# Kernel optimization log

Hardware: AMD Instinct MI355X
Metric: run time of the kernel (lower is better)

Reference implementation:

```python
import jax, jax.numpy as jnp
import numpy as np

N, IN, OUT = 8192, 4096, 4096
GROUP = 4
ACT_BITS = 8


def setup_inputs() -> dict:
    key = jax.random.key(0)
    k_x, k_w, k_b = jax.random.split(key, 3)
    input = jax.random.normal(k_x, (N, IN), dtype=jnp.float32)
    # ternary weights in {-1, 0, +1}, stored as float for compute
    weight = jax.random.randint(k_w, (OUT, IN), -1, 2).astype(jnp.float32)
    weight_scale = jnp.ones((1,), dtype=jnp.float32) * 0.02
    bias = jax.random.normal(k_b, (OUT,), dtype=jnp.float32) * 0.01
    return {"input": input, "weight": weight, "weight_scale": weight_scale, "bias": bias}


def reference(input, weight, weight_scale, bias):
    n, in_f = input.shape
    out_f = weight.shape[0]
    qmax = 2 ** (ACT_BITS - 1) - 1  # 127
    # absmax activation quantization (inference path)
    act_scale = jnp.abs(input).max() / qmax
    x_q = jnp.clip(jnp.round(input / act_scale), -(qmax + 1), qmax)
    # LUT path math: per 4-wide group, contribution = sum(w_group) * mean(x_group)
    g = in_f // GROUP
    x_mean = x_q.reshape(n, g, GROUP).mean(axis=-1)          # [N, G]
    w_sum = weight.reshape(out_f, g, GROUP).sum(axis=-1)     # [OUT, G]
    out = jnp.einsum('ng,og->no', x_mean, w_sum)
    out = out * weight_scale * act_scale + bias
    return out
```

## Files before the change

### kernel.cpp

```cpp
#include <hip/hip_runtime.h>
#include <hip/hip_bf16.h>

#define NROWS 8192
#define INF   4096
#define OUTF  4096
#define G     1024

typedef _Float16 f16x8 __attribute__((ext_vector_type(8)));
typedef float    f32x4 __attribute__((ext_vector_type(4)));

__global__ void absmax_kernel(const float4* __restrict__ x, int n4,
                              unsigned int* __restrict__ out_bits) {
    float m = 0.f;
    for (int i = blockIdx.x * blockDim.x + threadIdx.x; i < n4;
         i += gridDim.x * blockDim.x) {
        float4 v = x[i];
        m = fmaxf(m, fmaxf(fmaxf(fabsf(v.x), fabsf(v.y)),
                           fmaxf(fabsf(v.z), fabsf(v.w))));
    }
    for (int off = 32; off; off >>= 1)
        m = fmaxf(m, __shfl_down(m, off));
    __shared__ float wm[4];
    int lane = threadIdx.x & 63, wave = threadIdx.x >> 6;
    if (lane == 0) wm[wave] = m;
    __syncthreads();
    if (threadIdx.x == 0) {
        float bm = fmaxf(fmaxf(wm[0], wm[1]), fmaxf(wm[2], wm[3]));
        atomicMax(out_bits, __float_as_uint(bm));
    }
}

__global__ void quant_kernel(const float4* __restrict__ x,
                             _Float16* __restrict__ xs,
                             const unsigned int* __restrict__ max_bits,
                             int ngroups) {
    int i = blockIdx.x * blockDim.x + threadIdx.x;
    if (i >= ngroups) return;
    float s = __uint_as_float(*max_bits) * (1.0f / 127.0f);
    float4 v = x[i];
    float q0 = fminf(fmaxf(rintf(v.x / s), -128.f), 127.f);
    float q1 = fminf(fmaxf(rintf(v.y / s), -128.f), 127.f);
    float q2 = fminf(fmaxf(rintf(v.z / s), -128.f), 127.f);
    float q3 = fminf(fmaxf(rintf(v.w / s), -128.f), 127.f);
    xs[i] = (_Float16)(q0 + q1 + q2 + q3);
}

__global__ void wsum_kernel(const float4* __restrict__ w,
                            _Float16* __restrict__ ws,
                            int ngroups) {
    int i = blockIdx.x * blockDim.x + threadIdx.x;
    if (i >= ngroups) return;
    float4 v = w[i];
    ws[i] = (_Float16)(v.x + v.y + v.z + v.w);
}

#define TILE 128
#define BK   32

__device__ __forceinline__ void async_copy16(const void* g, void* l) {
    __builtin_amdgcn_global_load_lds(
        (const __attribute__((address_space(1))) unsigned int*)g,
        (__attribute__((address_space(3))) unsigned int*)l,
        16, 0, 0);
}

__global__ __launch_bounds__(256, 2) void gemm_kernel(
    const _Float16* __restrict__ A,
    const _Float16* __restrict__ B,
    const float* __restrict__ bias,
    const unsigned int* __restrict__ max_bits,
    const float* __restrict__ wscale,
    float* __restrict__ out) {

    __shared__ alignas(16) _Float16 As[TILE * BK];
    __shared__ alignas(16) _Float16 Bs[TILE * BK];

    const int t = threadIdx.x;
    const int lane = t & 63;
    const int wave = t >> 6;
    const int wm = (wave >> 1) * 64;
    const int wn = (wave & 1) * 64;

    const long rowA0 = (long)blockIdx.y * TILE;
    const long rowB0 = (long)blockIdx.x * TILE;

    f32x4 acc[4][4] = {};

    const int srow = (lane >> 2);
    const int scol = (lane & 3) * 8;

    for (int k0 = 0; k0 < G; k0 += BK) {
        __syncthreads();
        #pragma unroll
        for (int i = 0; i < 2; ++i) {
            const int c = wave + i * 4;
            const int row = c * 16 + srow;
            const _Float16* ga = A + (rowA0 + row) * (long)G + k0 + scol;
            const _Float16* gb = B + (rowB0 + row) * (long)G + k0 + scol;
            async_copy16(ga, As + c * 512);
            async_copy16(gb, Bs + c * 512);
        }
        __syncthreads();

        f16x8 af[4], bf[4];
        #pragma unroll
        for (int mi = 0; mi < 4; ++mi)
            af[mi] = *(const f16x8*)&As[(wm + mi * 16 + (lane & 15)) * BK + (lane >> 4) * 8];
        #pragma unroll
        for (int nj = 0; nj < 4; ++nj)
            bf[nj] = *(const f16x8*)&Bs[(wn + nj * 16 + (lane & 15)) * BK + (lane >> 4) * 8];

        #pragma unroll
        for (int mi = 0; mi < 4; ++mi)
            #pragma unroll
            for (int nj = 0; nj < 4; ++nj)
                acc[mi][nj] = __builtin_amdgcn_mfma_f32_16x16x32_f16(
                    af[mi], bf[nj], acc[mi][nj], 0, 0, 0);
    }

    const float scale = __uint_as_float(*max_bits) * (0.25f / 127.0f) * wscale[0];
    const int r0 = (int)rowA0 + wm + (lane >> 4) * 4;
    const int c0 = (int)rowB0 + wn + (lane & 15);
    #pragma unroll
    for (int nj = 0; nj < 4; ++nj) {
        const int col = c0 + nj * 16;
        const float b = bias[col];
        #pragma unroll
        for (int mi = 0; mi < 4; ++mi) {
            const int row = r0 + mi * 16;
            #pragma unroll
            for (int r = 0; r < 4; ++r)
                out[(long)(row + r) * OUTF + col] = acc[mi][nj][r] * scale + b;
        }
    }
}

extern "C" void kernel_launch(void* const* d_in, const int* in_sizes, int n_in,
                              void* d_out, int out_size, void* d_ws, size_t ws_size,
                              hipStream_t stream) {
    const float* input  = (const float*)d_in[0];
    const float* weight = (const float*)d_in[1];
    const float* wscale = (const float*)d_in[2];
    const float* bias   = (const float*)d_in[3];
    float* out = (float*)d_out;

    unsigned int* max_bits = (unsigned int*)d_ws;
    _Float16* x_sum = (_Float16*)((char*)d_ws + 256);
    _Float16* w_sum = (_Float16*)((char*)d_ws + 256 + (size_t)NROWS * G * 2);

    hipMemsetAsync(d_ws, 0, 4, stream);

    absmax_kernel<<<2048, 256, 0, stream>>>(
        (const float4*)input, NROWS * INF / 4, max_bits);

    quant_kernel<<<(NROWS * G + 255) / 256, 256, 0, stream>>>(
        (const float4*)input, x_sum, max_bits, NROWS * G);

    wsum_kernel<<<(OUTF * G + 255) / 256, 256, 0, stream>>>(
        (const float4*)weight, w_sum, OUTF * G);

    gemm_kernel<<<dim3(OUTF / TILE, NROWS / TILE), 256, 0, stream>>>(
        x_sum, w_sum, bias, max_bits, wscale, out);
}
```

Measured before the change: 385.1 us.

## Fuse absmax, quantize and weight-sum into one cooperative kernel; swizzle GEMM LDS

Replaces the memset plus three preprocessing kernels with a single cooperative-launch kernel. It computes per-block absmax partials, performs a grid-wide sync, reduces the partials redundantly in every block, then quantizes activations and sums weight groups in the same pass. This removes launch overhead and the atomic, and multiplies by an inverse scale instead of dividing. Separately, the GEMM uses an XOR swizzle on the LDS column for stores and fragment loads to reduce bank conflicts. The cost is a grid barrier and reliance on 1024 blocks fitting co-resident.

```diff
diff --git a/kernel.cpp b/kernel.cpp
--- a/kernel.cpp
+++ b/kernel.cpp
@@ -1,5 +1,8 @@
 #include <hip/hip_runtime.h>
 #include <hip/hip_bf16.h>
+#include <hip/hip_cooperative_groups.h>
+
+namespace cg = cooperative_groups;
 
 #define NROWS 8192
 #define INF   4096
@@ -9,49 +12,66 @@
 typedef _Float16 f16x8 __attribute__((ext_vector_type(8)));
 typedef float    f32x4 __attribute__((ext_vector_type(4)));
 
-__global__ void absmax_kernel(const float4* __restrict__ x, int n4,
-                              unsigned int* __restrict__ out_bits) {
+
+__global__ __launch_bounds__(256, 4) void prep_all(
+    const float4* __restrict__ x,
+    const float4* __restrict__ w,
+    float* __restrict__ act_scale_out,
+    float* __restrict__ partials,
+    _Float16* __restrict__ xs,
+    _Float16* __restrict__ ws) {
+
+    const int t   = threadIdx.x;
+    const int tid = blockIdx.x * 256 + t;
+    const int NT  = 1024 * 256;
+    const int lane = t & 63, wave = t >> 6;
+    __shared__ float red[4];
+
     float m = 0.f;
-    for (int i = blockIdx.x * blockDim.x + threadIdx.x; i < n4;
-         i += gridDim.x * blockDim.x) {
-        float4 v = x[i];
+    #pragma unroll 4
+    for (int it = 0; it < 32; ++it) {
+        float4 v = x[tid + it * NT];
         m = fmaxf(m, fmaxf(fmaxf(fabsf(v.x), fabsf(v.y)),
                            fmaxf(fabsf(v.z), fabsf(v.w))));
     }
     for (int off = 32; off; off >>= 1)
         m = fmaxf(m, __shfl_down(m, off));
-    __shared__ float wm[4];
-    int lane = threadIdx.x & 63, wave = threadIdx.x >> 6;
-    if (lane == 0) wm[wave] = m;
+    if (lane == 0) red[wave] = m;
     __syncthreads();
-    if (threadIdx.x == 0) {
-        float bm = fmaxf(fmaxf(wm[0], wm[1]), fmaxf(wm[2], wm[3]));
-        atomicMax(out_bits, __float_as_uint(bm));
+    if (t == 0)
+        partials[blockIdx.x] = fmaxf(fmaxf(red[0], red[1]), fmaxf(red[2], red[3]));
+    __threadfence();
+
+    cg::this_grid().sync();
+
+    __syncthreads();
+    float pm = fmaxf(fmaxf(partials[t], partials[t + 256]),
+                     fmaxf(partials[t + 512], partials[t + 768]));
+    for (int off = 32; off; off >>= 1)
+        pm = fmaxf(pm, __shfl_down(pm, off));
+    if (lane == 0) red[wave] = pm;
+    __syncthreads();
+    const float absmax = fmaxf(fmaxf(red[0], red[1]), fmaxf(red[2], red[3]));
+    const float s_inv = 127.0f / absmax;
+    if (tid == 0) act_scale_out[0] = absmax * (1.0f / 127.0f);
+
+    #pragma unroll 4
+    for (int it = 0; it < 32; ++it) {
+        int i = tid + it * NT;
+        float4 v = x[i];
+        float q0 = fminf(fmaxf(rintf(v.x * s_inv), -128.f), 127.f);
+        float q1 = fminf(fmaxf(rintf(v.y * s_inv), -128.f), 127.f);
+        float q2 = fminf(fmaxf(rintf(v.z * s_inv), -128.f), 127.f);
+        float q3 = fminf(fmaxf(rintf(v.w * s_inv), -128.f), 127.f);
+        xs[i] = (_Float16)(q0 + q1 + q2 + q3);
     }
-}
 
-__global__ void quant_kernel(const float4* __restrict__ x,
-                             _Float16* __restrict__ xs,
-                             const unsigned int* __restrict__ max_bits,
-                             int ngroups) {
-    int i = blockIdx.x * blockDim.x + threadIdx.x;
-    if (i >= ngroups) return;
-    float s = __uint_as_float(*max_bits) * (1.0f / 127.0f);
-    float4 v = x[i];
-    float q0 = fminf(fmaxf(rintf(v.x / s), -128.f), 127.f);
-    float q1 = fminf(fmaxf(rintf(v.y / s), -128.f), 127.f);
-    float q2 = fminf(fmaxf(rintf(v.z / s), -128.f), 127.f);
-    float q3 = fminf(fmaxf(rintf(v.w / s), -128.f), 127.f);
-    xs[i] = (_Float16)(q0 + q1 + q2 + q3);
-}
-
-__global__ void wsum_kernel(const float4* __restrict__ w,
-                            _Float16* __restrict__ ws,
-                            int ngroups) {
-    int i = blockIdx.x * blockDim.x + threadIdx.x;
-    if (i >= ngroups) return;
-    float4 v = w[i];
-    ws[i] = (_Float16)(v.x + v.y + v.z + v.w);
+    #pragma unroll 4
+    for (int it = 0; it < 16; ++it) {
+        int i = tid + it * NT;
+        float4 v = w[i];
+        ws[i] = (_Float16)(v.x + v.y + v.z + v.w);
+    }
 }
 
 #define TILE 128
@@ -68,7 +88,7 @@
     const _Float16* __restrict__ A,
     const _Float16* __restrict__ B,
     const float* __restrict__ bias,
-    const unsigned int* __restrict__ max_bits,
+    const float* __restrict__ scale_p,
     const float* __restrict__ wscale,
     float* __restrict__ out) {
 
@@ -86,8 +106,10 @@
 
     f32x4 acc[4][4] = {};
 
-    const int srow = (lane >> 2);
-    const int scol = (lane & 3) * 8;
+    const int srow = lane >> 2;
+    const int scol = ((lane & 3) ^ ((lane >> 3) & 3)) * 8;
+
+    const int kqs = (((lane >> 4) ^ ((lane >> 1) & 3)) * 8);
 
     for (int k0 = 0; k0 < G; k0 += BK) {
         __syncthreads();
@@ -105,10 +127,10 @@
         f16x8 af[4], bf[4];
         #pragma unroll
         for (int mi = 0; mi < 4; ++mi)
-            af[mi] = *(const f16x8*)&As[(wm + mi * 16 + (lane & 15)) * BK + (lane >> 4) * 8];
+            af[mi] = *(const f16x8*)&As[(wm + mi * 16 + (lane & 15)) * BK + kqs];
         #pragma unroll
         for (int nj = 0; nj < 4; ++nj)
-            bf[nj] = *(const f16x8*)&Bs[(wn + nj * 16 + (lane & 15)) * BK + (lane >> 4) * 8];
+            bf[nj] = *(const f16x8*)&Bs[(wn + nj * 16 + (lane & 15)) * BK + kqs];
 
         #pragma unroll
         for (int mi = 0; mi < 4; ++mi)
@@ -118,7 +140,7 @@
                     af[mi], bf[nj], acc[mi][nj], 0, 0, 0);
     }
 
-    const float scale = __uint_as_float(*max_bits) * (0.25f / 127.0f) * wscale[0];
+    const float scale = scale_p[0] * 0.25f * wscale[0];
     const int r0 = (int)rowA0 + wm + (lane >> 4) * 4;
     const int c0 = (int)rowB0 + wn + (lane & 15);
     #pragma unroll
@@ -144,21 +166,18 @@
     const float* bias   = (const float*)d_in[3];
     float* out = (float*)d_out;
 
-    unsigned int* max_bits = (unsigned int*)d_ws;
-    _Float16* x_sum = (_Float16*)((char*)d_ws + 256);
-    _Float16* w_sum = (_Float16*)((char*)d_ws + 256 + (size_t)NROWS * G * 2);
+    float* act_scale = (float*)d_ws;
+    float* partials  = (float*)((char*)d_ws + 256);
+    _Float16* x_sum  = (_Float16*)((char*)d_ws + 8192);
+    _Float16* w_sum  = (_Float16*)((char*)d_ws + 8192 + (size_t)NROWS * G * 2);
 
-    hipMemsetAsync(d_ws, 0, 4, stream);
-
-    absmax_kernel<<<2048, 256, 0, stream>>>(
-        (const float4*)input, NROWS * INF / 4, max_bits);
-
-    quant_kernel<<<(NROWS * G + 255) / 256, 256, 0, stream>>>(
-        (const float4*)input, x_sum, max_bits, NROWS * G);
-
-    wsum_kernel<<<(OUTF * G + 255) / 256, 256, 0, stream>>>(
-        (const float4*)weight, w_sum, OUTF * G);
+    const float4* x4 = (const float4*)input;
+    const float4* w4 = (const float4*)weight;
+    void* args[6] = { (void*)&x4, (void*)&w4, (void*)&act_scale,
+                      (void*)&partials, (void*)&x_sum, (void*)&w_sum };
+    hipLaunchCooperativeKernel((void*)prep_all, dim3(1024), dim3(256),
+                               args, 0, stream);
 
     gemm_kernel<<<dim3(OUTF / TILE, NROWS / TILE), 256, 0, stream>>>(
-        x_sum, w_sum, bias, max_bits, wscale, out);
+        x_sum, w_sum, bias, act_scale, wscale, out);
 }
```

Result: slower. 532.0 us (+38.2%).
